# Optimization experiments

Measured on AMD Instinct MI355X. Metric: run time of the kernel, lower is better.

## Reference

```python
import jax, jax.numpy as jnp
import numpy as np

B, S, D = 2, 4096, 1024
H = 16
HD = D // H  # 64


def setup_inputs() -> dict:
    key = jax.random.key(0)
    ks = jax.random.split(key, 5)
    scale = 1.0 / np.sqrt(D)
    return {
        "x": jax.random.normal(ks[0], (B, S, D), dtype=jnp.float32),
        "Wq": jax.random.normal(ks[1], (D, D), dtype=jnp.float32) * scale,
        "Wk": jax.random.normal(ks[2], (D, D), dtype=jnp.float32) * scale,
        "Wv": jax.random.normal(ks[3], (D, D), dtype=jnp.float32) * scale,
        "Wo": jax.random.normal(ks[4], (D, D), dtype=jnp.float32) * scale,
        "bo": jnp.zeros((D,), dtype=jnp.float32),
    }


def reference(x, Wq, Wk, Wv, Wo, bo):
    b, s, d = x.shape
    # Linear layers (torch layout: weight [out, in], y = x @ W.T)
    q = (x @ Wq.T).reshape(b, s, H, HD)
    k = (x @ Wk.T).reshape(b, s, H, HD)
    v = (x @ Wv.T).reshape(b, s, H, HD)
    # scores: [b, h, q, k]
    scores = jnp.einsum("bqhd,bkhd->bhqk", q, k)
    # causal mask (upper triangle above diagonal -> -inf)
    causal = jnp.triu(jnp.ones((s, s), dtype=bool), k=1)
    scores = jnp.where(causal[None, None], -jnp.inf, scores)
    weights = jax.nn.softmax(scores / np.sqrt(HD), axis=-1)  # dropout p=0.0 -> identity
    ctx = jnp.einsum("bhqk,bkhd->bqhd", weights, v).reshape(b, s, d)
    return ctx @ Wo.T + bo
```

## Files before the change

### kernel.cpp

```cpp
#include <hip/hip_runtime.h>
#include <stdint.h>
#include <stddef.h>

#define S_LEN 4096
#define NHEAD 16
#define HDIM 64
#define DMODEL 1024
#define NBATCH 2
#define LOG2E 1.4426950408889634f

typedef __attribute__((ext_vector_type(8))) short bf16x8;
typedef __attribute__((ext_vector_type(4))) float f32x4;
typedef __attribute__((ext_vector_type(16))) float f32x16;
typedef __attribute__((ext_vector_type(2))) unsigned int uint2v;
typedef __attribute__((ext_vector_type(4))) unsigned int uint4v;

__device__ inline unsigned short f2b(float f) {
    union { float f; unsigned int u; } x; x.f = f;
    unsigned int r = (x.u + 0x7fffu + ((x.u >> 16) & 1u)) >> 16;
    return (unsigned short)r;
}

__device__ inline unsigned cvt_pk_bf16(float lo, float hi) {
    unsigned r;
    asm("v_cvt_pk_bf16_f32 %0, %1, %2" : "=v"(r) : "v"(lo), "v"(hi));
    return r;
}

__device__ inline float exp_fast(float x) {
    float r;
    asm("v_exp_f32 %0, %1" : "=v"(r) : "v"(x));
    return r;
}

__device__ inline void gload_lds16(const void* g, void* l) {
    __builtin_amdgcn_global_load_lds((const __attribute__((address_space(1))) void*)g,
                                     (__attribute__((address_space(3))) void*)l,
                                     16, 0, 0);
}

__global__ void cvt_x(const float* __restrict__ in, unsigned short* __restrict__ out, int n4) {
    int i = blockIdx.x * 256 + threadIdx.x;
    if (i >= n4) return;
    float4 v = ((const float4*)in)[i];
    ushort4 o;
    o.x = f2b(v.x); o.y = f2b(v.y); o.z = f2b(v.z); o.w = f2b(v.w);
    ((ushort4*)out)[i] = o;
}

__global__ void cvt_w(const float* __restrict__ w0, const float* __restrict__ w1,
                      const float* __restrict__ w2, const float* __restrict__ w3,
                      unsigned short* __restrict__ dst) {
    int z = blockIdx.y;
    const float* src = (z == 0) ? w0 : (z == 1) ? w1 : (z == 2) ? w2 : w3;
    int i = blockIdx.x * 256 + threadIdx.x;
    float4 v = ((const float4*)src)[i];
    ushort4 o;
    o.x = f2b(v.x); o.y = f2b(v.y); o.z = f2b(v.z); o.w = f2b(v.w);
    ((ushort4*)(dst + (size_t)z * DMODEL * DMODEL))[i] = o;
}

__global__ __launch_bounds__(256, 2)
void gemm_qkv(const unsigned short* __restrict__ xb,
              const unsigned short* __restrict__ wqb,
              const unsigned short* __restrict__ wkb,
              const unsigned short* __restrict__ wvb,
              unsigned short* __restrict__ Qb,
              unsigned short* __restrict__ Kb,
              unsigned short* __restrict__ Vt,
              float qscale) {
    __shared__ unsigned short Asl[128 * 64];
    __shared__ unsigned short Bsl[128 * 64];
    const int tid  = threadIdx.x;
    const int lane = tid & 63;
    const int wid  = tid >> 6;
    const int wm   = (wid >> 1) * 64, wn = (wid & 1) * 64;
    const int lr   = lane & 15, lk = lane >> 4;
    const int z    = blockIdx.z;

    const unsigned short* A;
    const unsigned short* Bw;
    int m0, n0;
    if (z < 2) { A = xb; Bw = z ? wkb : wqb; m0 = blockIdx.x * 128; n0 = blockIdx.y * 128; }
    else       { A = wvb; Bw = xb;           m0 = blockIdx.y * 128; n0 = blockIdx.x * 128; }

    f32x4 acc[4][4];
#pragma unroll
    for (int i = 0; i < 4; ++i)
#pragma unroll
        for (int j = 0; j < 4; ++j) acc[i][j] = (f32x4){0.f, 0.f, 0.f, 0.f};

    for (int kt = 0; kt < DMODEL; kt += 64) {
#pragma unroll
        for (int i = 0; i < 4; ++i) {
            int c = i * 256 + tid;
            int r = c >> 3, gc = (c & 7) ^ (r & 7);
            gload_lds16(A + (size_t)(m0 + r) * DMODEL + kt + gc * 8, Asl + c * 8);
        }
#pragma unroll
        for (int i = 0; i < 4; ++i) {
            int c = i * 256 + tid;
            int r = c >> 3, gc = (c & 7) ^ (r & 7);
            gload_lds16(Bw + (size_t)(n0 + r) * DMODEL + kt + gc * 8, Bsl + c * 8);
        }
        __syncthreads();
#pragma unroll
        for (int kh = 0; kh < 2; ++kh) {
            int cl = kh * 4 + lk;
            bf16x8 af[4], bfr[4];
#pragma unroll
            for (int m = 0; m < 4; ++m) {
                int r = wm + m * 16 + lr;
                af[m] = *(const bf16x8*)(Asl + r * 64 + ((cl ^ (r & 7)) * 8));
            }
#pragma unroll
            for (int n = 0; n < 4; ++n) {
                int r = wn + n * 16 + lr;
                bfr[n] = *(const bf16x8*)(Bsl + r * 64 + ((cl ^ (r & 7)) * 8));
            }
#pragma unroll
            for (int m = 0; m < 4; ++m)
#pragma unroll
                for (int n = 0; n < 4; ++n)
                    acc[m][n] = __builtin_amdgcn_mfma_f32_16x16x32_bf16(af[m], bfr[n], acc[m][n], 0, 0, 0);
        }
        __syncthreads();
    }

#pragma unroll
    for (int m = 0; m < 4; ++m) {
#pragma unroll
        for (int n = 0; n < 4; ++n) {
            int gn = n0 + wn + n * 16 + lr;
#pragma unroll
            for (int r = 0; r < 4; ++r) {
                int gm = m0 + wm + m * 16 + lk * 4 + r;
                float v = acc[m][n][r];
                if (z == 0) {
                    int b = gm >> 12, s = gm & 4095, h = gn >> 6, hd = gn & 63;
                    Qb[((size_t)((b * NHEAD + h) * S_LEN + s)) * HDIM + hd] = f2b(v * qscale);
                } else if (z == 1) {
                    int b = gm >> 12, s = gm & 4095, h = gn >> 6, hd = gn & 63;
                    Kb[((size_t)((b * NHEAD + h) * S_LEN + s)) * HDIM + hd] = f2b(v);
                } else {
                    int h = gm >> 6, hd = gm & 63, b = gn >> 12, s = gn & 4095;
                    Vt[((size_t)((b * NHEAD + h) * HDIM + hd)) * S_LEN + s] = f2b(v);
                }
            }
        }
    }
}

__global__ __launch_bounds__(256, 2)
void gemm_out(const unsigned short* __restrict__ A,
              const unsigned short* __restrict__ Bw,
              float* __restrict__ out, const float* __restrict__ bias) {
    __shared__ unsigned short Asl[128 * 64];
    __shared__ unsigned short Bsl[128 * 64];
    const int tid  = threadIdx.x;
    const int lane = tid & 63;
    const int wid  = tid >> 6;
    const int wm   = (wid >> 1) * 64, wn = (wid & 1) * 64;
    const int lr   = lane & 15, lk = lane >> 4;
    const int m0   = blockIdx.x * 128, n0 = blockIdx.y * 128;

    f32x4 acc[4][4];
#pragma unroll
    for (int i = 0; i < 4; ++i)
#pragma unroll
        for (int j = 0; j < 4; ++j) acc[i][j] = (f32x4){0.f, 0.f, 0.f, 0.f};

    for (int kt = 0; kt < DMODEL; kt += 64) {
#pragma unroll
        for (int i = 0; i < 4; ++i) {
            int c = i * 256 + tid;
            int r = c >> 3, gc = (c & 7) ^ (r & 7);
            gload_lds16(A + (size_t)(m0 + r) * DMODEL + kt + gc * 8, Asl + c * 8);
        }
#pragma unroll
        for (int i = 0; i < 4; ++i) {
            int c = i * 256 + tid;
            int r = c >> 3, gc = (c & 7) ^ (r & 7);
            gload_lds16(Bw + (size_t)(n0 + r) * DMODEL + kt + gc * 8, Bsl + c * 8);
        }
        __syncthreads();
#pragma unroll
        for (int kh = 0; kh < 2; ++kh) {
            int cl = kh * 4 + lk;
            bf16x8 af[4], bfr[4];
#pragma unroll
            for (int m = 0; m < 4; ++m) {
                int r = wm + m * 16 + lr;
                af[m] = *(const bf16x8*)(Asl + r * 64 + ((cl ^ (r & 7)) * 8));
            }
#pragma unroll
            for (int n = 0; n < 4; ++n) {
                int r = wn + n * 16 + lr;
                bfr[n] = *(const bf16x8*)(Bsl + r * 64 + ((cl ^ (r & 7)) * 8));
            }
#pragma unroll
            for (int m = 0; m < 4; ++m)
#pragma unroll
                for (int n = 0; n < 4; ++n)
                    acc[m][n] = __builtin_amdgcn_mfma_f32_16x16x32_bf16(af[m], bfr[n], acc[m][n], 0, 0, 0);
        }
        __syncthreads();
    }
#pragma unroll
    for (int m = 0; m < 4; ++m)
#pragma unroll
        for (int n = 0; n < 4; ++n) {
            int gn = n0 + wn + n * 16 + lr;
#pragma unroll
            for (int r = 0; r < 4; ++r) {
                int gm = m0 + wm + m * 16 + lk * 4 + r;
                out[(size_t)gm * DMODEL + gn] = acc[m][n][r] + bias[gn];
            }
        }
}

__global__ __launch_bounds__(256)
void attn_fwd(const unsigned short* __restrict__ Q,
              const unsigned short* __restrict__ K,
              const unsigned short* __restrict__ Vt,
              unsigned short* __restrict__ ctx) {
    __shared__ unsigned short Kl[4][2048];
    __shared__ unsigned short Vl[4][2048];

    const int tid  = threadIdx.x;
    const int lane = tid & 63;
    const int w    = tid >> 6;
    const int l31  = lane & 31;
    const int hi   = lane >> 5;

    const int bid  = blockIdx.x;
    const int qt   = 31 - (bid >> 5);
    const int bh   = ((bid & 7) << 2) | ((bid >> 3) & 3);
    const int b    = bh >> 4, h = bh & 15;
    const int q0   = qt * 128;
    const int qw0  = q0 + w * 32;

    const unsigned short* Qh = Q  + (size_t)bh * S_LEN * HDIM;
    const unsigned short* Kh = K  + (size_t)bh * S_LEN * HDIM;
    const unsigned short* Vh = Vt + (size_t)bh * HDIM * S_LEN;

    const int sk   = tid >> 6;
    const int lS   = tid & 63;
    const int lS31 = lS & 31, hiS = lS >> 5;
    const unsigned short* kbase = Kh + (size_t)lS31 * HDIM + sk * 16 + hiS * 8;
    const unsigned short* vbase = Vh + (size_t)((sk >> 1) * 32 + lS31) * S_LEN + (sk & 1) * 16 + hiS * 8;

    bf16x8 qf[4];
    {
        const unsigned short* qrow = Qh + (size_t)(qw0 + l31) * HDIM + hi * 8;
#pragma unroll
        for (int s = 0; s < 4; ++s) qf[s] = *(const bf16x8*)(qrow + s * 16);
    }

    bf16x8 ones;
#pragma unroll
    for (int j = 0; j < 8; ++j) ones[j] = (short)0x3F80;

    f32x16 z16;
#pragma unroll
    for (int j = 0; j < 16; ++j) z16[j] = 0.f;

    const unsigned short* KL = &Kl[0][0] + lane * 8;
    const unsigned short* VL = &Vl[0][0] + lane * 8;

    f32x16 o0, o1, ls;
#pragma unroll
    for (int j = 0; j < 16; ++j) { o0[j] = 0.f; o1[j] = 0.f; ls[j] = 0.f; }

    const int nt = 4 * qt + 4;

    auto stage = [&](int buf, int t) {
        gload_lds16(kbase + (size_t)(t * 32) * HDIM, &Kl[buf][(size_t)tid * 8]);
        gload_lds16(vbase + t * 32, &Vl[buf][(size_t)tid * 8]);
    };

    auto packfrag = [&](const f32x16& v, int base) -> bf16x8 {
        unsigned a0 = cvt_pk_bf16(v[base + 0], v[base + 1]), a1 = cvt_pk_bf16(v[base + 2], v[base + 3]);
        unsigned b0 = cvt_pk_bf16(v[base + 4], v[base + 5]), b1 = cvt_pk_bf16(v[base + 6], v[base + 7]);
        uint2v r0 = __builtin_amdgcn_permlane32_swap(a0, b0, false, false);
        uint2v r1 = __builtin_amdgcn_permlane32_swap(a1, b1, false, false);
        uint4v f; f.x = r0.x; f.y = r1.x; f.z = r0.y; f.w = r1.y;
        return __builtin_bit_cast(bf16x8, f);
    };

    auto compute = [&](int buf, int kv0) {
        if (kv0 >= qw0 + 32) return;
        const unsigned short* KB = KL + buf * 2048;
        const unsigned short* VB = VL + buf * 2048;
        __builtin_amdgcn_s_setprio(1);
        f32x16 st = __builtin_amdgcn_mfma_f32_32x32x16_bf16(*(const bf16x8*)(KB + 0 * 512), qf[0], z16, 0, 0, 0);
        st = __builtin_amdgcn_mfma_f32_32x32x16_bf16(*(const bf16x8*)(KB + 1 * 512), qf[1], st, 0, 0, 0);
        st = __builtin_amdgcn_mfma_f32_32x32x16_bf16(*(const bf16x8*)(KB + 2 * 512), qf[2], st, 0, 0, 0);
        st = __builtin_amdgcn_mfma_f32_32x32x16_bf16(*(const bf16x8*)(KB + 3 * 512), qf[3], st, 0, 0, 0);
        __builtin_amdgcn_s_setprio(0);
        if (kv0 == qw0) {
#pragma unroll
            for (int j = 0; j < 16; ++j) {
                int roff = (j & 3) + 8 * (j >> 2) + 4 * hi;
                if (roff > l31) st[j] = -3e38f;
            }
        }
#pragma unroll
        for (int j = 0; j < 16; ++j) st[j] = exp_fast(st[j]);
        bf16x8 pa = packfrag(st, 0);
        bf16x8 pb = packfrag(st, 8);
        __builtin_amdgcn_s_setprio(1);
        ls = __builtin_amdgcn_mfma_f32_32x32x16_bf16(ones, pa, ls, 0, 0, 0);
        ls = __builtin_amdgcn_mfma_f32_32x32x16_bf16(ones, pb, ls, 0, 0, 0);
        o0 = __builtin_amdgcn_mfma_f32_32x32x16_bf16(*(const bf16x8*)(VB + 0 * 512), pa, o0, 0, 0, 0);
        o1 = __builtin_amdgcn_mfma_f32_32x32x16_bf16(*(const bf16x8*)(VB + 2 * 512), pa, o1, 0, 0, 0);
        o0 = __builtin_amdgcn_mfma_f32_32x32x16_bf16(*(const bf16x8*)(VB + 1 * 512), pb, o0, 0, 0, 0);
        o1 = __builtin_amdgcn_mfma_f32_32x32x16_bf16(*(const bf16x8*)(VB + 3 * 512), pb, o1, 0, 0, 0);
        __builtin_amdgcn_s_setprio(0);
    };

    stage(0, 0);
    stage(1, 1);
    stage(2, 2);
    for (int t = 0; t < nt - 2; ++t) {
        asm volatile("s_waitcnt vmcnt(4)" ::: "memory");
        asm volatile("s_barrier" ::: "memory");
        compute(t & 3, t * 32);
        if (t + 3 < nt) stage((t + 3) & 3, t + 3);
    }
    asm volatile("s_waitcnt vmcnt(2)" ::: "memory");
    asm volatile("s_barrier" ::: "memory");
    compute((nt - 2) & 3, (nt - 2) * 32);
    asm volatile("s_waitcnt vmcnt(0)" ::: "memory");
    asm volatile("s_barrier" ::: "memory");
    compute((nt - 1) & 3, (nt - 1) * 32);

    float inv = 1.f / ls[0];
    size_t sq = (size_t)q0 + w * 32 + l31;
    unsigned short* crow = ctx + ((size_t)b * S_LEN + sq) * DMODEL + h * HDIM;
#pragma unroll
    for (int quad = 0; quad < 4; ++quad) {
        int hdbase = quad * 8 + hi * 4;
        unsigned w0 = cvt_pk_bf16(o0[4 * quad] * inv, o0[4 * quad + 1] * inv);
        unsigned w1 = cvt_pk_bf16(o0[4 * quad + 2] * inv, o0[4 * quad + 3] * inv);
        *(unsigned long long*)(crow + hdbase) = ((unsigned long long)w1 << 32) | w0;
        unsigned w2 = cvt_pk_bf16(o1[4 * quad] * inv, o1[4 * quad + 1] * inv);
        unsigned w3 = cvt_pk_bf16(o1[4 * quad + 2] * inv, o1[4 * quad + 3] * inv);
        *(unsigned long long*)(crow + 32 + hdbase) = ((unsigned long long)w3 << 32) | w2;
    }
}

extern "C" void kernel_launch(void* const* d_in, const int* in_sizes, int n_in,
                              void* d_out, int out_size, void* d_ws, size_t ws_size,
                              hipStream_t stream) {
    (void)in_sizes; (void)n_in; (void)out_size; (void)ws_size;
    const float* x  = (const float*)d_in[0];
    const float* Wq = (const float*)d_in[1];
    const float* Wk = (const float*)d_in[2];
    const float* Wv = (const float*)d_in[3];
    const float* Wo = (const float*)d_in[4];
    const float* bo = (const float*)d_in[5];

    unsigned short* ws  = (unsigned short*)d_ws;
    const size_t NTOK = (size_t)NBATCH * S_LEN;
    unsigned short* xb  = ws;
    unsigned short* wqb = xb  + NTOK * DMODEL;
    unsigned short* wkb = wqb + (size_t)DMODEL * DMODEL;
    unsigned short* wvb = wkb + (size_t)DMODEL * DMODEL;
    unsigned short* wob = wvb + (size_t)DMODEL * DMODEL;
    unsigned short* Qb  = wob + (size_t)DMODEL * DMODEL;
    unsigned short* Kb  = Qb  + NTOK * DMODEL;
    unsigned short* Vt  = Kb  + NTOK * DMODEL;
    unsigned short* ctx = xb;

    int n4x = (int)(NTOK * DMODEL / 4);
    cvt_x<<<(n4x + 255) / 256, 256, 0, stream>>>(x, xb, n4x);
    cvt_w<<<dim3(DMODEL * DMODEL / 4 / 256, 4), 256, 0, stream>>>(Wq, Wk, Wv, Wo, wqb);

    const float qscale = 0.125f * LOG2E;
    gemm_qkv<<<dim3(64, 8, 3), 256, 0, stream>>>(xb, wqb, wkb, wvb, Qb, Kb, Vt, qscale);

    attn_fwd<<<1024, 256, 0, stream>>>(Qb, Kb, Vt, ctx);

    gemm_out<<<dim3(64, 8), 256, 0, stream>>>(ctx, wob, (float*)d_out, bo);
}
```

Before: 205.9 us.

## Split attention KV range across two blocks and add a combine kernel

Each query tile's causal KV range is split into two blocks at roughly a one-third point, doubling the grid from 1024 to 2048 blocks. Each half writes its unnormalised partial output as bf16 plus its row sum, and a new combine kernel adds the two halves and normalises. The goal is more parallelism and better load balance across CUs for the triangular workload. The cost is extra partial-result traffic, an extra launch, and a double-rounding step through bf16. The software pipeline also drops from 4 LDS buffers with 3-deep prefetch to 2 buffers with a __syncthreads per tile.

```diff
diff --git a/kernel.cpp b/kernel.cpp
--- a/kernel.cpp
+++ b/kernel.cpp
@@ -19,6 +19,10 @@
     union { float f; unsigned int u; } x; x.f = f;
     unsigned int r = (x.u + 0x7fffu + ((x.u >> 16) & 1u)) >> 16;
     return (unsigned short)r;
+}
+
+__device__ inline float b2f(unsigned short u) {
+    union { unsigned int u; float f; } x; x.u = ((unsigned int)u) << 16; return x.f;
 }
 
 __device__ inline unsigned cvt_pk_bf16(float lo, float hi) {
@@ -223,9 +227,10 @@
 void attn_fwd(const unsigned short* __restrict__ Q,
               const unsigned short* __restrict__ K,
               const unsigned short* __restrict__ Vt,
-              unsigned short* __restrict__ ctx) {
-    __shared__ unsigned short Kl[4][2048];
-    __shared__ unsigned short Vl[4][2048];
+              unsigned short* __restrict__ Opart,
+              float* __restrict__ lspart) {
+    __shared__ unsigned short Kl[2][2048];
+    __shared__ unsigned short Vl[2][2048];
 
     const int tid  = threadIdx.x;
     const int lane = tid & 63;
@@ -233,20 +238,21 @@
     const int l31  = lane & 31;
     const int hi   = lane >> 5;
 
-    const int bid  = blockIdx.x;
-    const int qt   = 31 - (bid >> 5);
-    const int bh   = ((bid & 7) << 2) | ((bid >> 3) & 3);
-    const int b    = bh >> 4, h = bh & 15;
-    const int q0   = qt * 128;
-    const int qw0  = q0 + w * 32;
+    const int bid   = blockIdx.x;
+    const int split = bid >> 10;
+    const int inner = bid & 1023;
+    const int qt    = 31 - (inner >> 5);
+    const int bh    = ((inner & 7) << 2) | ((inner >> 3) & 3);
+    const int b     = bh >> 4, h = bh & 15;
+    const int q0    = qt * 128;
+    const int qw0   = q0 + w * 32;
 
     const unsigned short* Qh = Q  + (size_t)bh * S_LEN * HDIM;
     const unsigned short* Kh = K  + (size_t)bh * S_LEN * HDIM;
     const unsigned short* Vh = Vt + (size_t)bh * HDIM * S_LEN;
 
     const int sk   = tid >> 6;
-    const int lS   = tid & 63;
-    const int lS31 = lS & 31, hiS = lS >> 5;
+    const int lS31 = tid & 31, hiS = (tid >> 5) & 1;
     const unsigned short* kbase = Kh + (size_t)lS31 * HDIM + sk * 16 + hiS * 8;
     const unsigned short* vbase = Vh + (size_t)((sk >> 1) * 32 + lS31) * S_LEN + (sk & 1) * 16 + hiS * 8;
 
@@ -272,7 +278,10 @@
 #pragma unroll
     for (int j = 0; j < 16; ++j) { o0[j] = 0.f; o1[j] = 0.f; ls[j] = 0.f; }
 
-    const int nt = 4 * qt + 4;
+    const int nt  = 4 * qt + 4;
+    const int ntA = (4 * qt + 5) / 3;
+    const int t_lo = split ? ntA : 0;
+    const int t_hi = split ? nt  : ntA;
 
     auto stage = [&](int buf, int t) {
         gload_lds16(kbase + (size_t)(t * 32) * HDIM, &Kl[buf][(size_t)tid * 8]);
@@ -319,35 +328,53 @@
         __builtin_amdgcn_s_setprio(0);
     };
 
-    stage(0, 0);
-    stage(1, 1);
-    stage(2, 2);
-    for (int t = 0; t < nt - 2; ++t) {
-        asm volatile("s_waitcnt vmcnt(4)" ::: "memory");
-        asm volatile("s_barrier" ::: "memory");
-        compute(t & 3, t * 32);
-        if (t + 3 < nt) stage((t + 3) & 3, t + 3);
-    }
-    asm volatile("s_waitcnt vmcnt(2)" ::: "memory");
-    asm volatile("s_barrier" ::: "memory");
-    compute((nt - 2) & 3, (nt - 2) * 32);
-    asm volatile("s_waitcnt vmcnt(0)" ::: "memory");
-    asm volatile("s_barrier" ::: "memory");
-    compute((nt - 1) & 3, (nt - 1) * 32);
-
-    float inv = 1.f / ls[0];
-    size_t sq = (size_t)q0 + w * 32 + l31;
-    unsigned short* crow = ctx + ((size_t)b * S_LEN + sq) * DMODEL + h * HDIM;
+    const int n = t_hi - t_lo;
+    stage(0, t_lo);
+    __syncthreads();
+    int cur = 0;
+    for (int i = 0; i < n; ++i) {
+        if (i + 1 < n) stage(cur ^ 1, t_lo + i + 1);
+        compute(cur, (t_lo + i) * 32);
+        __syncthreads();
+        cur ^= 1;
+    }
+
+    const size_t row = (size_t)b * S_LEN + q0 + w * 32 + l31;
+    unsigned short* crow = Opart + (size_t)split * 8192 * DMODEL + row * DMODEL + h * HDIM;
 #pragma unroll
     for (int quad = 0; quad < 4; ++quad) {
         int hdbase = quad * 8 + hi * 4;
-        unsigned w0 = cvt_pk_bf16(o0[4 * quad] * inv, o0[4 * quad + 1] * inv);
-        unsigned w1 = cvt_pk_bf16(o0[4 * quad + 2] * inv, o0[4 * quad + 3] * inv);
+        unsigned w0 = cvt_pk_bf16(o0[4 * quad], o0[4 * quad + 1]);
+        unsigned w1 = cvt_pk_bf16(o0[4 * quad + 2], o0[4 * quad + 3]);
         *(unsigned long long*)(crow + hdbase) = ((unsigned long long)w1 << 32) | w0;
-        unsigned w2 = cvt_pk_bf16(o1[4 * quad] * inv, o1[4 * quad + 1] * inv);
-        unsigned w3 = cvt_pk_bf16(o1[4 * quad + 2] * inv, o1[4 * quad + 3] * inv);
+        unsigned w2 = cvt_pk_bf16(o1[4 * quad], o1[4 * quad + 1]);
+        unsigned w3 = cvt_pk_bf16(o1[4 * quad + 2], o1[4 * quad + 3]);
         *(unsigned long long*)(crow + 32 + hdbase) = ((unsigned long long)w3 << 32) | w2;
     }
+    if (hi == 0)
+        lspart[(size_t)split * 8192 * NHEAD + row * NHEAD + h] = ls[0];
+}
+
+__global__ __launch_bounds__(256)
+void combine(const unsigned short* __restrict__ Opart,
+             const float* __restrict__ lspart,
+             unsigned short* __restrict__ ctx) {
+    int i = blockIdx.x * 256 + threadIdx.x;
+    int row = i >> 7;
+    int c8  = (i & 127) << 3;
+    int h   = c8 >> 6;
+    float l = lspart[(size_t)row * NHEAD + h] + lspart[(size_t)8192 * NHEAD + (size_t)row * NHEAD + h];
+    float inv = 1.f / l;
+    bf16x8 a = *(const bf16x8*)(Opart + (size_t)row * DMODEL + c8);
+    bf16x8 bb = *(const bf16x8*)(Opart + (size_t)8192 * DMODEL + (size_t)row * DMODEL + c8);
+    uint4v r;
+#pragma unroll
+    for (int j = 0; j < 4; ++j) {
+        float f0 = (b2f((unsigned short)a[2 * j])     + b2f((unsigned short)bb[2 * j]))     * inv;
+        float f1 = (b2f((unsigned short)a[2 * j + 1]) + b2f((unsigned short)bb[2 * j + 1])) * inv;
+        r[j] = cvt_pk_bf16(f0, f1);
+    }
+    *(uint4v*)(ctx + (size_t)row * DMODEL + c8) = r;
 }
 
 extern "C" void kernel_launch(void* const* d_in, const int* in_sizes, int n_in,
@@ -371,6 +398,8 @@
     unsigned short* Qb  = wob + (size_t)DMODEL * DMODEL;
     unsigned short* Kb  = Qb  + NTOK * DMODEL;
     unsigned short* Vt  = Kb  + NTOK * DMODEL;
+    unsigned short* Op  = Vt  + NTOK * DMODEL;
+    float*          lsp = (float*)(Op + 2 * NTOK * DMODEL);
     unsigned short* ctx = xb;
 
     int n4x = (int)(NTOK * DMODEL / 4);
@@ -380,7 +409,8 @@
     const float qscale = 0.125f * LOG2E;
     gemm_qkv<<<dim3(64, 8, 3), 256, 0, stream>>>(xb, wqb, wkb, wvb, Qb, Kb, Vt, qscale);
 
-    attn_fwd<<<1024, 256, 0, stream>>>(Qb, Kb, Vt, ctx);
+    attn_fwd<<<2048, 256, 0, stream>>>(Qb, Kb, Vt, Op, lsp);
+    combine<<<(int)(NTOK * DMODEL / 8 / 256), 256, 0, stream>>>(Op, lsp, ctx);
 
     gemm_out<<<dim3(64, 8), 256, 0, stream>>>(ctx, wob, (float*)d_out, bo);
 }
```

Result: slower. 233.4 us (+13.3%).
